# Kernel optimization log

Hardware: AMD Instinct MI355X
Metric: run time of the kernel (lower is better)

The kernel has to match this reference:

```python
import jax, jax.numpy as jnp
import numpy as np

B = 256
N_FACTS = 20
LQ = 16
LF = 16
E = 128
H = 256
DICT = 50000
GIN = 3 * H + 40  # 808
G_OUT = 256
F_OUT = 32


def setup_inputs() -> dict:
    key = jax.random.key(0)
    ks = iter(jax.random.split(key, 32))
    def w(shape, s=0.05):
        return jax.random.normal(next(ks), shape, jnp.float32) * s
    inp = {}
    inp["question_batch"] = jax.random.randint(next(ks), (B, LQ), 0, DICT + 1)
    inp["facts_batch"] = jax.random.randint(next(ks), (B * N_FACTS, LF), 0, DICT + 1)
    inp["embedding"] = w((DICT + 1, E))
    for nm in ("q", "f"):
        inp[f"Wih_{nm}"] = w((4 * H, E))
        inp[f"Whh_{nm}"] = w((4 * H, H))
        inp[f"bih_{nm}"] = jnp.zeros((4 * H,), jnp.float32)
        inp[f"bhh_{nm}"] = jnp.zeros((4 * H,), jnp.float32)
    g_dims = [GIN, 256, 256, 256, G_OUT]
    for i in range(4):
        inp[f"g_W{i}"] = w((g_dims[i + 1], g_dims[i]))
        inp[f"g_b{i}"] = jnp.zeros((g_dims[i + 1],), jnp.float32)
    f_dims = [G_OUT, 256, 512, F_OUT]
    for i in range(3):
        inp[f"f_W{i}"] = w((f_dims[i + 1], f_dims[i]))
        inp[f"f_b{i}"] = jnp.zeros((f_dims[i + 1],), jnp.float32)
    return inp


def lstm_final_hidden(x, Wih, Whh, bih, bhh):
    # x: [N, T, E] -> final hidden state h_T: [N, H] (PyTorch gate order i,f,g,o)
    n = x.shape[0]
    h0 = jnp.zeros((n, H), x.dtype)
    c0 = jnp.zeros((n, H), x.dtype)
    def step(carry, xt):
        h, c = carry
        gates = xt @ Wih.T + h @ Whh.T + bih + bhh  # [N, 4H]
        i, f, g, o = jnp.split(gates, 4, axis=-1)
        i = jax.nn.sigmoid(i); f = jax.nn.sigmoid(f); o = jax.nn.sigmoid(o)
        g = jnp.tanh(g)
        c = f * c + i * g
        h = o * jnp.tanh(c)
        return (h, c), None
    (h, c), _ = jax.lax.scan(step, (h0, c0), jnp.swapaxes(x, 0, 1))
    return h


def mlp(x, Ws, bs):
    # relu after every layer incl. output (mlp_tanh=False), dropout off (eval)
    for W, b in zip(Ws, bs):
        x = jax.nn.relu(x @ W.T + b)
    return x


def reference(question_batch, facts_batch, embedding,
              Wih_q, Whh_q, bih_q, bhh_q,
              Wih_f, Whh_f, bih_f, bhh_f,
              g_W0, g_b0, g_W1, g_b1, g_W2, g_b2, g_W3, g_b3,
              f_W0, f_b0, f_W1, f_b1, f_W2, f_b2):
    q_emb = embedding[question_batch]          # [B, LQ, E]
    f_emb = embedding[facts_batch]             # [B*N, LF, E]
    qh = lstm_final_hidden(q_emb, Wih_q, Whh_q, bih_q, bhh_q)   # [B, H]
    fh = lstm_final_hidden(f_emb, Wih_f, Whh_f, bih_f, bhh_f)   # [B*N, H]
    fh = fh.reshape(B, N_FACTS, H)
    sep = jnp.eye(20, dtype=fh.dtype)[:N_FACTS]                 # [N, 20]
    fh = jnp.concatenate([fh, jnp.broadcast_to(sep, (B, N_FACTS, 20))], axis=2)  # [B, N, H+20]
    # pairwise: oi cycles facts fast, oj repeats each fact N times (matches torch repeat/view)
    oi = jnp.tile(fh, (1, N_FACTS, 1))                           # [B, N*N, H+20]
    oj = jnp.repeat(fh, N_FACTS, axis=1)                         # [B, N*N, H+20]
    qr = jnp.broadcast_to(qh[:, None, :], (B, N_FACTS * N_FACTS, H))
    pair = jnp.concatenate([oi, oj, qr], axis=2)                 # [B, N*N, 3H+40]
    rel = mlp(pair.reshape(-1, GIN), (g_W0, g_W1, g_W2, g_W3), (g_b0, g_b1, g_b2, g_b3))
    rel_sum = rel.reshape(B, N_FACTS * N_FACTS, G_OUT).sum(axis=1)  # [B, G_OUT]
    out = mlp(rel_sum, (f_W0, f_W1, f_W2), (f_b0, f_b1, f_b2))      # [B, F_OUT]
    return out
```

## Files before the change

### kernel.cpp

```cpp
#include <hip/hip_runtime.h>
#include <math.h>

typedef __attribute__((ext_vector_type(8))) short short8;
typedef __attribute__((ext_vector_type(4))) float f32x4;
typedef __attribute__((ext_vector_type(4))) unsigned short u16x4;

#define NBQ 256
#define NBF 5120
#define MROWS 5376
#define E_ 128
#define H_ 256
#define DICTP1 50001
#define GIN_ 808

__device__ __forceinline__ unsigned short f2bf(float x) {
    unsigned int u = __float_as_uint(x);
    u += 0x7fffu + ((u >> 16) & 1u);
    return (unsigned short)(u >> 16);
}
__device__ __forceinline__ float bf2f(unsigned short b) {
    return __uint_as_float(((unsigned int)b) << 16);
}
__device__ __forceinline__ float sigmoidf_(float x) { return 1.0f / (1.0f + expf(-x)); }

__device__ __forceinline__ void gload16(const void* g, void* l) {
    __builtin_amdgcn_global_load_lds((const __attribute__((address_space(1))) void*)g,
                                     (__attribute__((address_space(3))) void*)l, 16, 0, 0);
}
__device__ __forceinline__ short8 frag128(const unsigned char* base, int row, int ko) {
    return *reinterpret_cast<const short8*>(base + (row << 7) + ((ko << 1) ^ ((row & 7) << 4)));
}
__device__ __forceinline__ short8 frag512(const unsigned char* base, int row, int ko) {
    return *reinterpret_cast<const short8*>(base + (row << 9) + ((ko << 1) ^ ((row & 7) << 4)));
}

__global__ __launch_bounds__(256) void lstm_step(
    const int* __restrict__ qidx, const int* __restrict__ fidx,
    const unsigned short* __restrict__ embb,
    const unsigned short* __restrict__ Wq, const unsigned short* __restrict__ Wf,
    const float* __restrict__ bsq, const float* __restrict__ bsf,
    const unsigned short* __restrict__ hr, unsigned short* __restrict__ hw,
    float* __restrict__ c, int t)
{
    __shared__ __align__(16) unsigned char Ash[16384];
    __shared__ __align__(16) unsigned char Bsh[16384];
    const int tid = threadIdx.x, lane = tid & 63, widx = tid >> 6;
    const int wr = widx >> 1, wc = widx & 1;
    const int gr = blockIdx.x * 128, bc = blockIdx.y;
    const bool isq = (gr < NBQ);
    const unsigned short* W = isq ? Wq : Wf;
    const float* bs = isq ? bsq : bsf;
    const int rsub = lane >> 3, cgrp = lane & 7;
    f32x4 acc[4][4] = {};
    for (int kt = 0; kt < 384; kt += 64) {
        #pragma unroll
        for (int j = 0; j < 4; ++j) {
            const int ch = (widx << 2) + j;
            const int r = (ch << 3) + rsub;
            const int ce = (cgrp ^ (r & 7)) << 3;
            const int n = gr + r;
            const unsigned short* asrc;
            if (kt < E_) {
                const int tok = isq ? qidx[(n << 4) + t] : fidx[((n - NBQ) << 4) + t];
                asrc = embb + (size_t)tok * E_ + kt + ce;
            } else {
                asrc = hr + (size_t)n * H_ + (kt - E_) + ce;
            }
            gload16(asrc, Ash + (ch << 10));
            const int grow = (((r & 63) >> 4) << 8) + (bc << 5) + ((r >> 6) << 4) + (r & 15);
            gload16(W + (size_t)grow * 384 + kt + ce, Bsh + (ch << 10));
        }
        __syncthreads();
        #pragma unroll
        for (int kk = 0; kk < 64; kk += 32) {
            const int ko = kk + ((lane >> 4) << 3);
            short8 af[4], bfr[4];
            #pragma unroll
            for (int i = 0; i < 4; ++i) {
                af[i]  = frag128(Ash, wr * 64 + i * 16 + (lane & 15), ko);
                bfr[i] = frag128(Bsh, wc * 64 + i * 16 + (lane & 15), ko);
            }
            #pragma unroll
            for (int mi = 0; mi < 4; ++mi)
                #pragma unroll
                for (int ni = 0; ni < 4; ++ni)
                    acc[mi][ni] = __builtin_amdgcn_mfma_f32_16x16x32_bf16(af[mi], bfr[ni], acc[mi][ni], 0, 0, 0);
        }
        __syncthreads();
    }
    const int hcol = (bc << 5) + (wc << 4) + (lane & 15);
    float bsv[4];
    #pragma unroll
    for (int g = 0; g < 4; ++g) bsv[g] = bs[(g << 8) + hcol];
    #pragma unroll
    for (int mi = 0; mi < 4; ++mi) {
        #pragma unroll
        for (int rg = 0; rg < 4; ++rg) {
            const int m = gr + wr * 64 + mi * 16 + ((lane >> 4) << 2) + rg;
            const float iv = sigmoidf_(acc[mi][0][rg] + bsv[0]);
            const float fv = sigmoidf_(acc[mi][1][rg] + bsv[1]);
            const float gv = tanhf(acc[mi][2][rg] + bsv[2]);
            const float ov = sigmoidf_(acc[mi][3][rg] + bsv[3]);
            const size_t idx = (size_t)m * H_ + hcol;
            const float cn = fv * c[idx] + iv * gv;
            c[idx] = cn;
            hw[idx] = f2bf(ov * tanhf(cn));
        }
    }
}

__global__ __launch_bounds__(256) void g123sum(
    const float* __restrict__ UV, const float* __restrict__ Q0,
    const float* __restrict__ sepU, const float* __restrict__ sepV,
    const unsigned short* __restrict__ gw1b, const float* __restrict__ gb1,
    const unsigned short* __restrict__ gw2b, const float* __restrict__ gb2,
    const unsigned short* __restrict__ gw3b, const float* __restrict__ gb3,
    float* __restrict__ rel_sum)
{
    __shared__ __align__(16) unsigned char actA[16384];
    __shared__ __align__(16) unsigned char actB[16384];
    __shared__ __align__(16) unsigned char Wsh[32768];
    const int tid = threadIdx.x, lane = tid & 63, widx = tid >> 6;
    const int grow0 = blockIdx.x << 5;
    {
        const int r = tid >> 3;
        const int c0 = (tid & 7) << 5;
        const int grow = grow0 + r;
        const int b = grow / 400;
        const int rem = grow - b * 400;
        const int oi = rem % 20, oj = rem / 20;
        const float* up = UV + ((size_t)(b * 20 + oi) << 9);
        const float* vp = UV + ((size_t)(b * 20 + oj) << 9) + 256;
        const float* qp = Q0 + ((size_t)b << 8);
        const float* sup = sepU + (oi << 8);
        const float* svp = sepV + (oj << 8);
        #pragma unroll
        for (int cc = 0; cc < 32; cc += 4) {
            const int c = c0 + cc;
            const float4 u = *(const float4*)(up + c);
            const float4 v = *(const float4*)(vp + c);
            const float4 q = *(const float4*)(qp + c);
            const float4 su = *(const float4*)(sup + c);
            const float4 sv = *(const float4*)(svp + c);
            u16x4 pk;
            pk.x = f2bf(fmaxf(u.x + v.x + q.x + su.x + sv.x, 0.f));
            pk.y = f2bf(fmaxf(u.y + v.y + q.y + su.y + sv.y, 0.f));
            pk.z = f2bf(fmaxf(u.z + v.z + q.z + su.z + sv.z, 0.f));
            pk.w = f2bf(fmaxf(u.w + v.w + q.w + su.w + sv.w, 0.f));
            *(u16x4*)(actA + (r << 9) + (((c << 1) ^ ((r & 7) << 4)))) = pk;
        }
    }
    #pragma unroll 1
    for (int L = 0; L < 3; ++L) {
        const unsigned char* ain = (L & 1) ? actB : actA;
        unsigned char* aout = (L & 1) ? actA : actB;
        const unsigned short* Wp = (L == 0) ? gw1b : (L == 1) ? gw2b : gw3b;
        const float* bl = (L == 0) ? gb1 : (L == 1) ? gb2 : gb3;
        f32x4 acc[2][4] = {};
        for (int kc = 0; kc < 4; ++kc) {
            #pragma unroll
            for (int j = 0; j < 8; ++j) {
                const int unit = (widx << 3) + j;
                const int r = (unit << 3) + (lane >> 3);
                const int ce = ((lane & 7) ^ (r & 7)) << 3;
                gload16(Wp + ((size_t)r << 8) + (kc << 6) + ce, Wsh + (unit << 10));
            }
            __syncthreads();
            #pragma unroll
            for (int ks = 0; ks < 2; ++ks) {
                const int kof = (ks << 5) + ((lane >> 4) << 3);
                const int kcol = (kc << 6) + kof;
                short8 af[2], bfr[4];
                af[0] = frag512(ain, (lane & 15), kcol);
                af[1] = frag512(ain, 16 + (lane & 15), kcol);
                #pragma unroll
                for (int ni = 0; ni < 4; ++ni)
                    bfr[ni] = frag128(Wsh, (widx << 6) + (ni << 4) + (lane & 15), kof);
                #pragma unroll
                for (int mi = 0; mi < 2; ++mi)
                    #pragma unroll
                    for (int ni = 0; ni < 4; ++ni)
                        acc[mi][ni] = __builtin_amdgcn_mfma_f32_16x16x32_bf16(af[mi], bfr[ni], acc[mi][ni], 0, 0, 0);
            }
            __syncthreads();
        }
        float bv[4];
        #pragma unroll
        for (int ni = 0; ni < 4; ++ni) bv[ni] = bl[(widx << 6) + (ni << 4) + (lane & 15)];
        if (L < 2) {
            #pragma unroll
            for (int mi = 0; mi < 2; ++mi)
                #pragma unroll
                for (int ni = 0; ni < 4; ++ni)
                    #pragma unroll
                    for (int rg4 = 0; rg4 < 4; ++rg4) {
                        const float v = fmaxf(acc[mi][ni][rg4] + bv[ni], 0.f);
                        const int row = (mi << 4) + ((lane >> 4) << 2) + rg4;
                        const int col = (widx << 6) + (ni << 4) + (lane & 15);
                        *(unsigned short*)(aout + (row << 9) + (((col << 1) ^ ((row & 7) << 4)))) = f2bf(v);
                    }
        } else {
            const int bstart = grow0 / 400;
            const int rsplit = (bstart + 1) * 400 - grow0;
            const int b1 = (bstart < 255) ? bstart + 1 : 255;
            #pragma unroll
            for (int ni = 0; ni < 4; ++ni) {
                float s0 = 0.f, s1 = 0.f;
                #pragma unroll
                for (int mi = 0; mi < 2; ++mi)
                    #pragma unroll
                    for (int rg4 = 0; rg4 < 4; ++rg4) {
                        const int row = (mi << 4) + ((lane >> 4) << 2) + rg4;
                        const float v = fmaxf(acc[mi][ni][rg4] + bv[ni], 0.f);
                        if (row < rsplit) s0 += v; else s1 += v;
                    }
                s0 += __shfl_xor(s0, 16); s0 += __shfl_xor(s0, 32);
                s1 += __shfl_xor(s1, 16); s1 += __shfl_xor(s1, 32);
                if (lane < 16) {
                    const int col = (widx << 6) + (ni << 4) + lane;
                    atomicAdd(&rel_sum[(bstart << 8) + col], s0);
                    atomicAdd(&rel_sum[(b1 << 8) + col], s1);
                }
            }
        }
    }
}

template <int RELU, int OBF>
__global__ __launch_bounds__(256) void mm_bf16(
    const unsigned short* __restrict__ A, int lda,
    const unsigned short* __restrict__ B, int ldb,
    const float* __restrict__ bias,
    float* __restrict__ Cf, unsigned short* __restrict__ Cb, int ldc, int K)
{
    __shared__ __align__(16) unsigned char Ash[16384];
    __shared__ __align__(16) unsigned char Bsh[16384];
    const int tid = threadIdx.x, lane = tid & 63, widx = tid >> 6;
    const int wr = widx >> 1, wc = widx & 1;
    const int gr = blockIdx.x * 128, gc = blockIdx.y * 128;
    const int rsub = lane >> 3, cgrp = lane & 7;
    f32x4 acc[4][4] = {};
    for (int kt = 0; kt < K; kt += 64) {
        #pragma unroll
        for (int j = 0; j < 4; ++j) {
            const int ch = (widx << 2) + j;
            const int r = (ch << 3) + rsub;
            const int ce = (cgrp ^ (r & 7)) << 3;
            gload16(A + (size_t)(gr + r) * lda + kt + ce, Ash + (ch << 10));
            gload16(B + (size_t)(gc + r) * ldb + kt + ce, Bsh + (ch << 10));
        }
        __syncthreads();
        #pragma unroll
        for (int kk = 0; kk < 64; kk += 32) {
            const int ko = kk + ((lane >> 4) << 3);
            short8 af[4], bfr[4];
            #pragma unroll
            for (int i = 0; i < 4; ++i) {
                af[i]  = frag128(Ash, wr * 64 + i * 16 + (lane & 15), ko);
                bfr[i] = frag128(Bsh, wc * 64 + i * 16 + (lane & 15), ko);
            }
            #pragma unroll
            for (int mi = 0; mi < 4; ++mi)
                #pragma unroll
                for (int ni = 0; ni < 4; ++ni)
                    acc[mi][ni] = __builtin_amdgcn_mfma_f32_16x16x32_bf16(af[mi], bfr[ni], acc[mi][ni], 0, 0, 0);
        }
        __syncthreads();
    }
    const int rq = (lane >> 4) << 2, cl = lane & 15;
    #pragma unroll
    for (int ni = 0; ni < 4; ++ni) {
        const int n = gc + wc * 64 + ni * 16 + cl;
        const float bv = bias ? bias[n] : 0.f;
        #pragma unroll
        for (int mi = 0; mi < 4; ++mi) {
            #pragma unroll
            for (int rg = 0; rg < 4; ++rg) {
                const int m = gr + wr * 64 + mi * 16 + rq + rg;
                float v = acc[mi][ni][rg] + bv;
                if (RELU) v = fmaxf(v, 0.f);
                if (OBF) Cb[(size_t)m * ldc + n] = f2bf(v);
                else     Cf[(size_t)m * ldc + n] = v;
            }
        }
    }
}

__global__ void cvt_bf16(const float* __restrict__ s, unsigned short* __restrict__ d, int n) {
    for (int i = blockIdx.x * blockDim.x + threadIdx.x; i < n; i += gridDim.x * blockDim.x)
        d[i] = f2bf(s[i]);
}

__global__ void pack_lstm_w(const float* __restrict__ Wih, const float* __restrict__ Whh,
                            const float* __restrict__ bih, const float* __restrict__ bhh,
                            unsigned short* __restrict__ Wc, float* __restrict__ bsum) {
    const int r = blockIdx.x;
    const int cx = threadIdx.x;
    const float v = (cx < E_) ? Wih[r * E_ + cx] : Whh[r * H_ + cx - E_];
    Wc[r * 384 + cx] = f2bf(v);
    if (cx == 0) bsum[r] = bih[r] + bhh[r];
}

__global__ __launch_bounds__(256) void pack_w0(const float* __restrict__ gW0, const float* __restrict__ gb0,
                                               unsigned short* __restrict__ W0ab, unsigned short* __restrict__ W0c,
                                               float* __restrict__ sepU, float* __restrict__ sepV) {
    const int idx = blockIdx.x * 256 + threadIdx.x;
    if (idx < 131072) {
        const int r = idx >> 8, cc = idx & 255;
        const float v = (r < 256) ? gW0[(size_t)r * GIN_ + cc] : gW0[(size_t)(r - 256) * GIN_ + 276 + cc];
        W0ab[idx] = f2bf(v);
    } else if (idx < 196608) {
        const int l = idx - 131072;
        const int r = l >> 8, cc = l & 255;
        W0c[l] = f2bf(gW0[(size_t)r * GIN_ + 552 + cc]);
    } else if (idx < 201728) {
        const int l = idx - 196608;
        const int i = l >> 8, j = l & 255;
        sepU[l] = gW0[(size_t)j * GIN_ + 256 + i] + gb0[j];
    } else {
        const int l = idx - 201728;
        const int i = l >> 8, j = l & 255;
        sepV[l] = gW0[(size_t)j * GIN_ + 532 + i];
    }
}

template <int RELU>
__global__ __launch_bounds__(256) void gemm_nt(
    const float* __restrict__ A, int lda,
    const float* __restrict__ B, int ldb,
    const float* __restrict__ bias,
    float* __restrict__ C, int ldc,
    int M, int N, int K)
{
    __shared__ float As[16][68];
    __shared__ float Bs[16][68];
    const int tid = threadIdx.x;
    const int tx = tid & 15, ty = tid >> 4;
    const int lrow = tid >> 2;
    const int lk = (tid & 3) << 2;
    const int gr = blockIdx.x * 64, gc = blockIdx.y * 64;
    const int ar = gr + lrow;
    const int brr = gc + lrow;
    const float* __restrict__ arow = A + (size_t)ar * lda;
    const float* __restrict__ brow = B + (size_t)brr * ldb;
    const bool aval = ar < M, bval = brr < N;
    float acc[4][4] = {};
    for (int k0 = 0; k0 < K; k0 += 16) {
        float4 a4 = make_float4(0.f, 0.f, 0.f, 0.f), b4 = make_float4(0.f, 0.f, 0.f, 0.f);
        if (aval) a4 = *reinterpret_cast<const float4*>(arow + k0 + lk);
        if (bval) b4 = *reinterpret_cast<const float4*>(brow + k0 + lk);
        As[lk + 0][lrow] = a4.x; As[lk + 1][lrow] = a4.y; As[lk + 2][lrow] = a4.z; As[lk + 3][lrow] = a4.w;
        Bs[lk + 0][lrow] = b4.x; Bs[lk + 1][lrow] = b4.y; Bs[lk + 2][lrow] = b4.z; Bs[lk + 3][lrow] = b4.w;
        __syncthreads();
        #pragma unroll
        for (int kk = 0; kk < 16; ++kk) {
            float a0 = As[kk][ty * 4 + 0], a1 = As[kk][ty * 4 + 1], a2 = As[kk][ty * 4 + 2], a3 = As[kk][ty * 4 + 3];
            float b0 = Bs[kk][tx * 4 + 0], b1 = Bs[kk][tx * 4 + 1], b2 = Bs[kk][tx * 4 + 2], b3 = Bs[kk][tx * 4 + 3];
            acc[0][0] += a0 * b0; acc[0][1] += a0 * b1; acc[0][2] += a0 * b2; acc[0][3] += a0 * b3;
            acc[1][0] += a1 * b0; acc[1][1] += a1 * b1; acc[1][2] += a1 * b2; acc[1][3] += a1 * b3;
            acc[2][0] += a2 * b0; acc[2][1] += a2 * b1; acc[2][2] += a2 * b2; acc[2][3] += a2 * b3;
            acc[3][0] += a3 * b0; acc[3][1] += a3 * b1; acc[3][2] += a3 * b2; acc[3][3] += a3 * b3;
        }
        __syncthreads();
    }
    #pragma unroll
    for (int i = 0; i < 4; ++i)
        #pragma unroll
        for (int jj = 0; jj < 4; ++jj) {
            const int r = gr + ty * 4 + i, cc = gc + tx * 4 + jj;
            if (r < M && cc < N) {
                float v = acc[i][jj] + (bias ? bias[cc] : 0.f);
                if (RELU) v = fmaxf(v, 0.f);
                C[(size_t)r * ldc + cc] = v;
            }
        }
}

extern "C" void kernel_launch(void* const* d_in, const int* in_sizes, int n_in,
                              void* d_out, int out_size, void* d_ws, size_t ws_size,
                              hipStream_t stream)
{
    const int* qidx = (const int*)d_in[0];
    const int* fidx = (const int*)d_in[1];
    const float* emb = (const float*)d_in[2];
    const float* Wih_q = (const float*)d_in[3];
    const float* Whh_q = (const float*)d_in[4];
    const float* bih_q = (const float*)d_in[5];
    const float* bhh_q = (const float*)d_in[6];
    const float* Wih_f = (const float*)d_in[7];
    const float* Whh_f = (const float*)d_in[8];
    const float* bih_f = (const float*)d_in[9];
    const float* bhh_f = (const float*)d_in[10];
    const float* gW0 = (const float*)d_in[11];
    const float* gb0 = (const float*)d_in[12];
    const float* gW1 = (const float*)d_in[13];
    const float* gb1 = (const float*)d_in[14];
    const float* gW2 = (const float*)d_in[15];
    const float* gb2 = (const float*)d_in[16];
    const float* gW3 = (const float*)d_in[17];
    const float* gb3 = (const float*)d_in[18];
    const float* fW0 = (const float*)d_in[19];
    const float* fb0 = (const float*)d_in[20];
    const float* fW1 = (const float*)d_in[21];
    const float* fb1 = (const float*)d_in[22];
    const float* fW2 = (const float*)d_in[23];
    const float* fb2 = (const float*)d_in[24];
    float* out = (float*)d_out;

    char* w = (char*)d_ws;
    float* c = (float*)w;                      w += (size_t)MROWS * H_ * 4;
    unsigned short* hb0 = (unsigned short*)w;  w += (size_t)MROWS * H_ * 2;
    unsigned short* hb1 = (unsigned short*)w;  w += (size_t)MROWS * H_ * 2;
    unsigned short* embb = (unsigned short*)w; w += (size_t)DICTP1 * E_ * 2;
    unsigned short* Wq = (unsigned short*)w;   w += (size_t)1024 * 384 * 2;
    unsigned short* Wf = (unsigned short*)w;   w += (size_t)1024 * 384 * 2;
    float* bsq = (float*)w;                    w += 1024 * 4;
    float* bsf = (float*)w;                    w += 1024 * 4;
    unsigned short* W0ab = (unsigned short*)w; w += (size_t)512 * 256 * 2;
    unsigned short* W0c = (unsigned short*)w;  w += (size_t)256 * 256 * 2;
    unsigned short* gw1b = (unsigned short*)w; w += (size_t)256 * 256 * 2;
    unsigned short* gw2b = (unsigned short*)w; w += (size_t)256 * 256 * 2;
    unsigned short* gw3b = (unsigned short*)w; w += (size_t)256 * 256 * 2;
    float* sepU = (float*)w;                   w += 20 * 256 * 4;
    float* sepV = (float*)w;                   w += 20 * 256 * 4;
    float* UV = (float*)w;                     w += (size_t)NBF * 512 * 4;
    float* Q0 = (float*)w;                     w += (size_t)NBQ * H_ * 4;
    float* rel_sum = (float*)w;                w += (size_t)NBQ * H_ * 4;
    float* fout1 = (float*)w;                  w += (size_t)NBQ * 256 * 4;
    float* fout2 = (float*)w;                  w += (size_t)NBQ * 512 * 4;

    (void)hipMemsetAsync(c, 0, (size_t)MROWS * H_ * 4 + (size_t)MROWS * H_ * 2, stream);
    (void)hipMemsetAsync(rel_sum, 0, (size_t)NBQ * H_ * 4, stream);

    cvt_bf16<<<2048, 256, 0, stream>>>(emb, embb, DICTP1 * E_);
    pack_lstm_w<<<1024, 384, 0, stream>>>(Wih_q, Whh_q, bih_q, bhh_q, Wq, bsq);
    pack_lstm_w<<<1024, 384, 0, stream>>>(Wih_f, Whh_f, bih_f, bhh_f, Wf, bsf);
    pack_w0<<<808, 256, 0, stream>>>(gW0, gb0, W0ab, W0c, sepU, sepV);
    cvt_bf16<<<64, 256, 0, stream>>>(gW1, gw1b, 256 * 256);
    cvt_bf16<<<64, 256, 0, stream>>>(gW2, gw2b, 256 * 256);
    cvt_bf16<<<64, 256, 0, stream>>>(gW3, gw3b, 256 * 256);

    for (int t = 0; t < 16; ++t) {
        const unsigned short* hr = (t & 1) ? hb1 : hb0;
        unsigned short* hw = (t & 1) ? hb0 : hb1;
        lstm_step<<<dim3(MROWS / 128, 8), 256, 0, stream>>>(
            qidx, fidx, embb, Wq, Wf, bsq, bsf, hr, hw, c, t);
    }

    const unsigned short* fh = hb0 + (size_t)NBQ * H_;
    mm_bf16<0, 0><<<dim3(NBF / 128, 4), 256, 0, stream>>>(fh, H_, W0ab, H_, nullptr, UV, nullptr, 512, H_);
    mm_bf16<0, 0><<<dim3(NBQ / 128, 2), 256, 0, stream>>>(hb0, H_, W0c, H_, nullptr, Q0, nullptr, H_, H_);

    g123sum<<<3200, 256, 0, stream>>>(UV, Q0, sepU, sepV, gw1b, gb1, gw2b, gb2, gw3b, gb3, rel_sum);

    gemm_nt<1><<<dim3(NBQ / 64, 256 / 64), 256, 0, stream>>>(rel_sum, H_, fW0, H_, fb0, fout1, H_, NBQ, 256, H_);
    gemm_nt<1><<<dim3(NBQ / 64, 512 / 64), 256, 0, stream>>>(fout1, 256, fW1, 256, fb1, fout2, 512, NBQ, 512, 256);
    gemm_nt<1><<<dim3(NBQ / 64, 1), 256, 0, stream>>>(fout2, 512, fW2, 512, fb2, out, 32, NBQ, 32, 512);
}
```

Before: 635.5 us.

## Replace per-timestep LSTM launches with persistent cooperative kernel and register cell state

The 16 per-timestep LSTM kernel launches become one cooperative persistent kernel of 168 blocks with 512 threads, separated by grid-wide syncs. Each block owns a fixed 256-row by 32-hidden-column tile. The cell state c stays in registers across timesteps instead of being read and written in global memory each step. This removes launch overhead and the c traffic, but runs only 168 blocks at one block per CU, so it depends on grid.sync latency and lower parallelism.

New measurement: 952.1 us. 49.8% more time.

```diff
diff --git a/kernel.cpp b/kernel.cpp
--- a/kernel.cpp
+++ b/kernel.cpp
@@ -1,5 +1,8 @@
 #include <hip/hip_runtime.h>
+#include <hip/hip_cooperative_groups.h>
 #include <math.h>
+
+namespace cg = cooperative_groups;
 
 typedef __attribute__((ext_vector_type(8))) short short8;
 typedef __attribute__((ext_vector_type(4))) float f32x4;
@@ -18,9 +21,6 @@
     u += 0x7fffu + ((u >> 16) & 1u);
     return (unsigned short)(u >> 16);
 }
-__device__ __forceinline__ float bf2f(unsigned short b) {
-    return __uint_as_float(((unsigned int)b) << 16);
-}
 __device__ __forceinline__ float sigmoidf_(float x) { return 1.0f / (1.0f + expf(-x)); }
 
 __device__ __forceinline__ void gload16(const void* g, void* l) {
@@ -34,78 +34,96 @@
     return *reinterpret_cast<const short8*>(base + (row << 9) + ((ko << 1) ^ ((row & 7) << 4)));
 }
 
-__global__ __launch_bounds__(256) void lstm_step(
+__global__ __launch_bounds__(512, 1) void lstm_persist(
     const int* __restrict__ qidx, const int* __restrict__ fidx,
     const unsigned short* __restrict__ embb,
     const unsigned short* __restrict__ Wq, const unsigned short* __restrict__ Wf,
     const float* __restrict__ bsq, const float* __restrict__ bsf,
-    const unsigned short* __restrict__ hr, unsigned short* __restrict__ hw,
-    float* __restrict__ c, int t)
+    unsigned short* __restrict__ hb0, unsigned short* __restrict__ hb1)
 {
-    __shared__ __align__(16) unsigned char Ash[16384];
+    cg::grid_group gridg = cg::this_grid();
+    __shared__ __align__(16) unsigned char Ash[32768];
     __shared__ __align__(16) unsigned char Bsh[16384];
     const int tid = threadIdx.x, lane = tid & 63, widx = tid >> 6;
     const int wr = widx >> 1, wc = widx & 1;
-    const int gr = blockIdx.x * 128, bc = blockIdx.y;
-    const bool isq = (gr < NBQ);
+    const int rgp = blockIdx.x >> 3, cgp = blockIdx.x & 7;
+    const int row0 = rgp << 8;
+    const bool isq = (rgp == 0);
     const unsigned short* W = isq ? Wq : Wf;
     const float* bs = isq ? bsq : bsf;
-    const int rsub = lane >> 3, cgrp = lane & 7;
-    f32x4 acc[4][4] = {};
-    for (int kt = 0; kt < 384; kt += 64) {
-        #pragma unroll
-        for (int j = 0; j < 4; ++j) {
-            const int ch = (widx << 2) + j;
-            const int r = (ch << 3) + rsub;
-            const int ce = (cgrp ^ (r & 7)) << 3;
-            const int n = gr + r;
-            const unsigned short* asrc;
-            if (kt < E_) {
-                const int tok = isq ? qidx[(n << 4) + t] : fidx[((n - NBQ) << 4) + t];
-                asrc = embb + (size_t)tok * E_ + kt + ce;
-            } else {
-                asrc = hr + (size_t)n * H_ + (kt - E_) + ce;
-            }
-            gload16(asrc, Ash + (ch << 10));
-            const int grow = (((r & 63) >> 4) << 8) + (bc << 5) + ((r >> 6) << 4) + (r & 15);
-            gload16(W + (size_t)grow * 384 + kt + ce, Bsh + (ch << 10));
-        }
-        __syncthreads();
-        #pragma unroll
-        for (int kk = 0; kk < 64; kk += 32) {
-            const int ko = kk + ((lane >> 4) << 3);
-            short8 af[4], bfr[4];
-            #pragma unroll
-            for (int i = 0; i < 4; ++i) {
-                af[i]  = frag128(Ash, wr * 64 + i * 16 + (lane & 15), ko);
-                bfr[i] = frag128(Bsh, wc * 64 + i * 16 + (lane & 15), ko);
-            }
-            #pragma unroll
-            for (int mi = 0; mi < 4; ++mi)
-                #pragma unroll
-                for (int ni = 0; ni < 4; ++ni)
-                    acc[mi][ni] = __builtin_amdgcn_mfma_f32_16x16x32_bf16(af[mi], bfr[ni], acc[mi][ni], 0, 0, 0);
-        }
-        __syncthreads();
-    }
-    const int hcol = (bc << 5) + (wc << 4) + (lane & 15);
+    const int hcol = (cgp << 5) + (wc << 4) + (lane & 15);
     float bsv[4];
     #pragma unroll
     for (int g = 0; g < 4; ++g) bsv[g] = bs[(g << 8) + hcol];
+    float creg[16];
     #pragma unroll
-    for (int mi = 0; mi < 4; ++mi) {
-        #pragma unroll
-        for (int rg = 0; rg < 4; ++rg) {
-            const int m = gr + wr * 64 + mi * 16 + ((lane >> 4) << 2) + rg;
-            const float iv = sigmoidf_(acc[mi][0][rg] + bsv[0]);
-            const float fv = sigmoidf_(acc[mi][1][rg] + bsv[1]);
-            const float gv = tanhf(acc[mi][2][rg] + bsv[2]);
-            const float ov = sigmoidf_(acc[mi][3][rg] + bsv[3]);
-            const size_t idx = (size_t)m * H_ + hcol;
-            const float cn = fv * c[idx] + iv * gv;
-            c[idx] = cn;
-            hw[idx] = f2bf(ov * tanhf(cn));
-        }
+    for (int i = 0; i < 16; ++i) creg[i] = 0.f;
+    const int sr = lane >> 3, sc = lane & 7;
+
+    const unsigned short* hr = hb0;
+    unsigned short* hw = hb1;
+    for (int t = 0; t < 16; ++t) {
+        f32x4 acc[4][4] = {};
+        for (int kc = 0; kc < 6; ++kc) {
+            #pragma unroll
+            for (int j = 0; j < 4; ++j) {
+                const int unit = (widx << 2) + j;
+                const int r = (unit << 3) + sr;
+                const int ce = (sc ^ (r & 7)) << 3;
+                const int n = row0 + r;
+                const unsigned short* src;
+                if (kc < 2) {
+                    const int tok = isq ? qidx[(n << 4) + t] : fidx[((n - NBQ) << 4) + t];
+                    src = embb + ((size_t)tok << 7) + (kc << 6) + ce;
+                } else {
+                    src = hr + ((size_t)n << 8) + ((kc - 2) << 6) + ce;
+                }
+                gload16(src, Ash + (unit << 10));
+            }
+            #pragma unroll
+            for (int j = 0; j < 2; ++j) {
+                const int unit = (widx << 1) + j;
+                const int r = (unit << 3) + sr;
+                const int ce = (sc ^ (r & 7)) << 3;
+                const int grow = ((r >> 5) << 8) + (cgp << 5) + (((r >> 4) & 1) << 4) + (r & 15);
+                gload16(W + (size_t)grow * 384 + (kc << 6) + ce, Bsh + (unit << 10));
+            }
+            __syncthreads();
+            #pragma unroll
+            for (int ks = 0; ks < 2; ++ks) {
+                const int ko = (ks << 5) + ((lane >> 4) << 3);
+                short8 af[4], bfr[4];
+                #pragma unroll
+                for (int i = 0; i < 4; ++i)
+                    af[i] = frag128(Ash, (wr << 6) + (i << 4) + (lane & 15), ko);
+                #pragma unroll
+                for (int i = 0; i < 4; ++i)
+                    bfr[i] = frag128(Bsh, (((i << 1) + wc) << 4) + (lane & 15), ko);
+                #pragma unroll
+                for (int mi = 0; mi < 4; ++mi)
+                    #pragma unroll
+                    for (int gi = 0; gi < 4; ++gi)
+                        acc[mi][gi] = __builtin_amdgcn_mfma_f32_16x16x32_bf16(af[mi], bfr[gi], acc[mi][gi], 0, 0, 0);
+            }
+            __syncthreads();
+        }
+        #pragma unroll
+        for (int mi = 0; mi < 4; ++mi) {
+            #pragma unroll
+            for (int rg4 = 0; rg4 < 4; ++rg4) {
+                const int ci = (mi << 2) + rg4;
+                const float iv = sigmoidf_(acc[mi][0][rg4] + bsv[0]);
+                const float fv = sigmoidf_(acc[mi][1][rg4] + bsv[1]);
+                const float gv = tanhf(acc[mi][2][rg4] + bsv[2]);
+                const float ov = sigmoidf_(acc[mi][3][rg4] + bsv[3]);
+                const float cn = fv * creg[ci] + iv * gv;
+                creg[ci] = cn;
+                const int m = row0 + (wr << 6) + (mi << 4) + ((lane >> 4) << 2) + rg4;
+                hw[((size_t)m << 8) + hcol] = f2bf(ov * tanhf(cn));
+            }
+        }
+        unsigned short* tmp = (unsigned short*)hr; hr = hw; hw = tmp;
+        if (t < 15) gridg.sync();
     }
 }
 
@@ -408,7 +426,6 @@
     float* out = (float*)d_out;
 
     char* w = (char*)d_ws;
-    float* c = (float*)w;                      w += (size_t)MROWS * H_ * 4;
     unsigned short* hb0 = (unsigned short*)w;  w += (size_t)MROWS * H_ * 2;
     unsigned short* hb1 = (unsigned short*)w;  w += (size_t)MROWS * H_ * 2;
     unsigned short* embb = (unsigned short*)w; w += (size_t)DICTP1 * E_ * 2;
@@ -429,7 +446,7 @@
     float* fout1 = (float*)w;                  w += (size_t)NBQ * 256 * 4;
     float* fout2 = (float*)w;                  w += (size_t)NBQ * 512 * 4;
 
-    (void)hipMemsetAsync(c, 0, (size_t)MROWS * H_ * 4 + (size_t)MROWS * H_ * 2, stream);
+    (void)hipMemsetAsync(hb0, 0, (size_t)MROWS * H_ * 2, stream);
     (void)hipMemsetAsync(rel_sum, 0, (size_t)NBQ * H_ * 4, stream);
 
     cvt_bf16<<<2048, 256, 0, stream>>>(emb, embb, DICTP1 * E_);
@@ -440,11 +457,10 @@
     cvt_bf16<<<64, 256, 0, stream>>>(gW2, gw2b, 256 * 256);
     cvt_bf16<<<64, 256, 0, stream>>>(gW3, gw3b, 256 * 256);
 
-    for (int t = 0; t < 16; ++t) {
-        const unsigned short* hr = (t & 1) ? hb1 : hb0;
-        unsigned short* hw = (t & 1) ? hb0 : hb1;
-        lstm_step<<<dim3(MROWS / 128, 8), 256, 0, stream>>>(
-            qidx, fidx, embb, Wq, Wf, bsq, bsf, hr, hw, c, t);
+    {
+        void* args[] = {(void*)&qidx, (void*)&fidx, (void*)&embb, (void*)&Wq, (void*)&Wf,
+                        (void*)&bsq, (void*)&bsf, (void*)&hb0, (void*)&hb1};
+        (void)hipLaunchCooperativeKernel((const void*)lstm_persist, dim3(168), dim3(512), args, 0, stream);
     }
 
     const unsigned short* fh = hb0 + (size_t)NBQ * H_;
```
